# Performance work log

Hardware: AMD Instinct MI355X
Metric: run time of the kernel (lower is better)

Reference implementation:

```python
import jax, jax.numpy as jnp
import numpy as np

RH, RW = 4, 4

def window_sum(x, rh, rw):
    # cumsum along H (axis 2)
    cum_h = jnp.cumsum(x, axis=2)
    wh = 2 * rh + 1
    top = cum_h[:, :, rh:wh, :]
    midh = cum_h[:, :, wh:, :] - cum_h[:, :, :-wh, :]
    bot = cum_h[:, :, -1:, :] - cum_h[:, :, -wh:-rh - 1, :]
    out = jnp.concatenate([top, midh, bot], axis=2)
    # cumsum along W (axis 3)
    cum_w = jnp.cumsum(out, axis=3)
    ww = 2 * rw + 1
    left = cum_w[:, :, :, rw:ww]
    midw = cum_w[:, :, :, ww:] - cum_w[:, :, :, :-ww]
    right = cum_w[:, :, :, -1:] - cum_w[:, :, :, -ww:-rw - 1]
    return jnp.concatenate([left, midw, right], axis=3)


def setup_inputs() -> dict:
    key = jax.random.key(0)
    x = jax.random.normal(key, (16, 3, 1024, 1024), dtype=jnp.float32)
    return {"x": x}


def reference(x):
    win_sum = window_sum(x, RH, RW)
    count = window_sum(jnp.ones_like(x), RH, RW)
    return win_sum / count
```

## Files before the change

### kernel.cpp

```cpp
#include <hip/hip_runtime.h>

#define HH 1024
#define WW 1024
#define BH 32
#define RAD 4
#define NSTRIP (HH / BH)

typedef float vfloat4 __attribute__((ext_vector_type(4)));

struct HS { float h0, h1, h2, h3; };

__device__ __forceinline__ HS hsum_row(const float* __restrict__ row, int c,
                                       bool first, bool last) {
    float4 b = *(const float4*)(row + c);
    float4 a, d;
    if (first) a = make_float4(0.f, 0.f, 0.f, 0.f);
    else       a = *(const float4*)(row + c - 4);
    if (last)  d = make_float4(0.f, 0.f, 0.f, 0.f);
    else       d = *(const float4*)(row + c + 4);
    HS h;
    h.h0 = ((a.x + a.y) + (a.z + a.w)) + ((b.x + b.y) + (b.z + b.w)) + d.x;
    h.h1 = h.h0 - a.x + d.y;
    h.h2 = h.h1 - a.y + d.z;
    h.h3 = h.h2 - a.z + d.w;
    return h;
}

#define STEP_FAST(J) do {                                                  \
    HS h = hsum_row(rowp, c, first, last);                                 \
    vs0 += h.h0 - ring[J].h0;                                              \
    vs1 += h.h1 - ring[J].h1;                                              \
    vs2 += h.h2 - ring[J].h2;                                              \
    vs3 += h.h3 - ring[J].h3;                                              \
    ring[J] = h;                                                           \
    vfloat4 o4 = {vs0 * w0, vs1 * w1, vs2 * w2, vs3 * w3};                 \
    __builtin_nontemporal_store(o4, (vfloat4*)(op + c));                   \
    rowp += WW; op += WW;                                                  \
} while (0)

#define STEP_GEN(J) do {                                                   \
    int rl = r + RAD;                                                      \
    HS h;                                                                  \
    if (rl < HH) h = hsum_row(xin + (size_t)rl * WW, c, first, last);      \
    else { h.h0 = 0.f; h.h1 = 0.f; h.h2 = 0.f; h.h3 = 0.f; }               \
    vs0 += h.h0 - ring[J].h0;                                              \
    vs1 += h.h1 - ring[J].h1;                                              \
    vs2 += h.h2 - ring[J].h2;                                              \
    vs3 += h.h3 - ring[J].h3;                                              \
    ring[J] = h;                                                           \
    int lo = r - RAD; if (lo < 0) lo = 0;                                  \
    int hi = r + RAD; if (hi > HH - 1) hi = HH - 1;                        \
    float ich = 1.0f / (float)(hi - lo + 1);                               \
    vfloat4 o4 = {vs0 * ich * sw[0], vs1 * ich * sw[1],                    \
                  vs2 * ich * sw[2], vs3 * ich * sw[3]};                   \
    __builtin_nontemporal_store(o4, (vfloat4*)(o + (size_t)r * WW + c));   \
    ++r;                                                                   \
} while (0)

__global__ __launch_bounds__(256, 4)
void box_kernel(const float* __restrict__ x, float* __restrict__ out) {
    const int tid = threadIdx.x;

    const int lin  = blockIdx.x + NSTRIP * blockIdx.y;
    const int nblk = NSTRIP * gridDim.y;
    const int cpx  = nblk >> 3;
    const int swz  = (lin & 7) * cpx + (lin >> 3);
    const int strip = swz & (NSTRIP - 1);
    const int img   = swz / NSTRIP;

    const int r0 = strip * BH;
    const int c  = tid * 4;
    const bool first = (tid == 0);
    const bool last  = (tid == 255);

    const float* __restrict__ xin = x + (size_t)img * (HH * WW);
    float* __restrict__ o = out + (size_t)img * (HH * WW);

    float sw[4];
#pragma unroll
    for (int j = 0; j < 4; ++j) {
        int cc = c + j;
        int lo = cc - RAD < 0 ? 0 : cc - RAD;
        int hi = cc + RAD > WW - 1 ? WW - 1 : cc + RAD;
        sw[j] = 1.0f / (float)(hi - lo + 1);
    }

    HS ring[9];
    float vs0 = 0.f, vs1 = 0.f, vs2 = 0.f, vs3 = 0.f;
#pragma unroll
    for (int k = 0; k < 9; ++k) {
        int rr = r0 - RAD - 1 + k;
        HS h;
        if (rr >= 0) h = hsum_row(xin + (size_t)rr * WW, c, first, last);
        else { h.h0 = 0.f; h.h1 = 0.f; h.h2 = 0.f; h.h3 = 0.f; }
        ring[k] = h;
        vs0 += h.h0; vs1 += h.h1; vs2 += h.h2; vs3 += h.h3;
    }

    const bool interior = (r0 >= RAD) && (r0 + BH + RAD <= HH);

    if (interior) {
        const float w0 = sw[0] * (1.0f / 9.0f);
        const float w1 = sw[1] * (1.0f / 9.0f);
        const float w2 = sw[2] * (1.0f / 9.0f);
        const float w3 = sw[3] * (1.0f / 9.0f);
        const float* __restrict__ rowp = xin + (size_t)(r0 + RAD) * WW;
        float* __restrict__ op = o + (size_t)r0 * WW;
#pragma unroll 1
        for (int chunk = 0; chunk < 3; ++chunk) {
            STEP_FAST(0); STEP_FAST(1); STEP_FAST(2); STEP_FAST(3); STEP_FAST(4);
            STEP_FAST(5); STEP_FAST(6); STEP_FAST(7); STEP_FAST(8);
        }
        STEP_FAST(0); STEP_FAST(1); STEP_FAST(2); STEP_FAST(3); STEP_FAST(4);
    } else {
        int r = r0;
#pragma unroll 1
        for (int chunk = 0; chunk < 3; ++chunk) {
            STEP_GEN(0); STEP_GEN(1); STEP_GEN(2); STEP_GEN(3); STEP_GEN(4);
            STEP_GEN(5); STEP_GEN(6); STEP_GEN(7); STEP_GEN(8);
        }
        STEP_GEN(0); STEP_GEN(1); STEP_GEN(2); STEP_GEN(3); STEP_GEN(4);
    }
}

extern "C" void kernel_launch(void* const* d_in, const int* in_sizes, int n_in,
                              void* d_out, int out_size, void* d_ws, size_t ws_size,
                              hipStream_t stream) {
    const float* x = (const float*)d_in[0];
    float* out = (float*)d_out;
    int n_images = in_sizes[0] / (HH * WW);
    dim3 grid(NSTRIP, n_images);
    dim3 block(256);
    box_kernel<<<grid, block, 0, stream>>>(x, out);
}
```

Baseline: 366.5 us.

## Prefetch input rows three steps ahead and double strip height

The interior loop now loads each row three steps before it is consumed, rotating through three register sets, so global-load latency overlaps with the running vertical sum. Strip height rises from 32 to 64 rows, which reduces halo rows re-read per output row and halves the block count. Launch bounds drop to 3 waves to make room for the extra registers, and output stores become plain stores instead of nontemporal ones. The trade-offs are lower occupancy, fewer blocks to spread across CUs, and different cache behaviour for the output writes.

```diff
diff --git a/kernel.cpp b/kernel.cpp
--- a/kernel.cpp
+++ b/kernel.cpp
@@ -2,22 +2,13 @@
 
 #define HH 1024
 #define WW 1024
-#define BH 32
+#define BH 64
 #define RAD 4
 #define NSTRIP (HH / BH)
 
-typedef float vfloat4 __attribute__((ext_vector_type(4)));
-
 struct HS { float h0, h1, h2, h3; };
 
-__device__ __forceinline__ HS hsum_row(const float* __restrict__ row, int c,
-                                       bool first, bool last) {
-    float4 b = *(const float4*)(row + c);
-    float4 a, d;
-    if (first) a = make_float4(0.f, 0.f, 0.f, 0.f);
-    else       a = *(const float4*)(row + c - 4);
-    if (last)  d = make_float4(0.f, 0.f, 0.f, 0.f);
-    else       d = *(const float4*)(row + c + 4);
+__device__ __forceinline__ HS hcompute(float4 a, float4 b, float4 d) {
     HS h;
     h.h0 = ((a.x + a.y) + (a.z + a.w)) + ((b.x + b.y) + (b.z + b.w)) + d.x;
     h.h1 = h.h0 - a.x + d.y;
@@ -26,23 +17,32 @@
     return h;
 }
 
-#define STEP_FAST(J) do {                                                  \
-    HS h = hsum_row(rowp, c, first, last);                                 \
+#define LOADROW(pa, pb, pd, rowptr) do {                                   \
+    pb = *(const float4*)((rowptr) + c);                                   \
+    pa = first ? z4 : *(const float4*)((rowptr) + c - 4);                  \
+    pd = last  ? z4 : *(const float4*)((rowptr) + c + 4);                  \
+} while (0)
+
+#define PSTEP(J, PX) do {                                                  \
+    HS h = hcompute(pa##PX, pb##PX, pd##PX);                               \
+    LOADROW(pa##PX, pb##PX, pd##PX, rowp); rowp += WW;                     \
     vs0 += h.h0 - ring[J].h0;                                              \
     vs1 += h.h1 - ring[J].h1;                                              \
     vs2 += h.h2 - ring[J].h2;                                              \
     vs3 += h.h3 - ring[J].h3;                                              \
     ring[J] = h;                                                           \
-    vfloat4 o4 = {vs0 * w0, vs1 * w1, vs2 * w2, vs3 * w3};                 \
-    __builtin_nontemporal_store(o4, (vfloat4*)(op + c));                   \
-    rowp += WW; op += WW;                                                  \
+    *(float4*)(op + c) = make_float4(vs0 * w0, vs1 * w1, vs2 * w2, vs3 * w3); \
+    op += WW;                                                              \
 } while (0)
 
-#define STEP_GEN(J) do {                                                   \
+#define GSTEP(J) do {                                                      \
     int rl = r + RAD;                                                      \
     HS h;                                                                  \
-    if (rl < HH) h = hsum_row(xin + (size_t)rl * WW, c, first, last);      \
-    else { h.h0 = 0.f; h.h1 = 0.f; h.h2 = 0.f; h.h3 = 0.f; }               \
+    if (rl < HH) {                                                         \
+        float4 a, b, d;                                                    \
+        LOADROW(a, b, d, xin + (size_t)rl * WW);                           \
+        h = hcompute(a, b, d);                                             \
+    } else { h.h0 = h.h1 = h.h2 = h.h3 = 0.f; }                            \
     vs0 += h.h0 - ring[J].h0;                                              \
     vs1 += h.h1 - ring[J].h1;                                              \
     vs2 += h.h2 - ring[J].h2;                                              \
@@ -51,13 +51,13 @@
     int lo = r - RAD; if (lo < 0) lo = 0;                                  \
     int hi = r + RAD; if (hi > HH - 1) hi = HH - 1;                        \
     float ich = 1.0f / (float)(hi - lo + 1);                               \
-    vfloat4 o4 = {vs0 * ich * sw[0], vs1 * ich * sw[1],                    \
-                  vs2 * ich * sw[2], vs3 * ich * sw[3]};                   \
-    __builtin_nontemporal_store(o4, (vfloat4*)(o + (size_t)r * WW + c));   \
+    *(float4*)(o + (size_t)r * WW + c) =                                   \
+        make_float4(vs0 * ich * sw[0], vs1 * ich * sw[1],                  \
+                    vs2 * ich * sw[2], vs3 * ich * sw[3]);                 \
     ++r;                                                                   \
 } while (0)
 
-__global__ __launch_bounds__(256, 4)
+__global__ __launch_bounds__(256, 3)
 void box_kernel(const float* __restrict__ x, float* __restrict__ out) {
     const int tid = threadIdx.x;
 
@@ -72,6 +72,7 @@
     const int c  = tid * 4;
     const bool first = (tid == 0);
     const bool last  = (tid == 255);
+    const float4 z4 = make_float4(0.f, 0.f, 0.f, 0.f);
 
     const float* __restrict__ xin = x + (size_t)img * (HH * WW);
     float* __restrict__ o = out + (size_t)img * (HH * WW);
@@ -91,8 +92,11 @@
     for (int k = 0; k < 9; ++k) {
         int rr = r0 - RAD - 1 + k;
         HS h;
-        if (rr >= 0) h = hsum_row(xin + (size_t)rr * WW, c, first, last);
-        else { h.h0 = 0.f; h.h1 = 0.f; h.h2 = 0.f; h.h3 = 0.f; }
+        if (rr >= 0) {
+            float4 a, b, d;
+            LOADROW(a, b, d, xin + (size_t)rr * WW);
+            h = hcompute(a, b, d);
+        } else { h.h0 = h.h1 = h.h2 = h.h3 = 0.f; }
         ring[k] = h;
         vs0 += h.h0; vs1 += h.h1; vs2 += h.h2; vs3 += h.h3;
     }
@@ -104,22 +108,29 @@
         const float w1 = sw[1] * (1.0f / 9.0f);
         const float w2 = sw[2] * (1.0f / 9.0f);
         const float w3 = sw[3] * (1.0f / 9.0f);
-        const float* __restrict__ rowp = xin + (size_t)(r0 + RAD) * WW;
-        float* __restrict__ op = o + (size_t)r0 * WW;
+
+        float4 pa0, pb0, pd0, pa1, pb1, pd1, pa2, pb2, pd2;
+        const float* rowp = xin + (size_t)(r0 + RAD) * WW;
+        LOADROW(pa0, pb0, pd0, rowp); rowp += WW;
+        LOADROW(pa1, pb1, pd1, rowp); rowp += WW;
+        LOADROW(pa2, pb2, pd2, rowp); rowp += WW;
+
+        float* op = o + (size_t)r0 * WW;
 #pragma unroll 1
-        for (int chunk = 0; chunk < 3; ++chunk) {
-            STEP_FAST(0); STEP_FAST(1); STEP_FAST(2); STEP_FAST(3); STEP_FAST(4);
-            STEP_FAST(5); STEP_FAST(6); STEP_FAST(7); STEP_FAST(8);
+        for (int chunk = 0; chunk < 7; ++chunk) {
+            PSTEP(0, 0); PSTEP(1, 1); PSTEP(2, 2);
+            PSTEP(3, 0); PSTEP(4, 1); PSTEP(5, 2);
+            PSTEP(6, 0); PSTEP(7, 1); PSTEP(8, 2);
         }
-        STEP_FAST(0); STEP_FAST(1); STEP_FAST(2); STEP_FAST(3); STEP_FAST(4);
+        PSTEP(0, 0);
     } else {
         int r = r0;
 #pragma unroll 1
-        for (int chunk = 0; chunk < 3; ++chunk) {
-            STEP_GEN(0); STEP_GEN(1); STEP_GEN(2); STEP_GEN(3); STEP_GEN(4);
-            STEP_GEN(5); STEP_GEN(6); STEP_GEN(7); STEP_GEN(8);
+        for (int chunk = 0; chunk < 7; ++chunk) {
+            GSTEP(0); GSTEP(1); GSTEP(2); GSTEP(3); GSTEP(4);
+            GSTEP(5); GSTEP(6); GSTEP(7); GSTEP(8);
         }
-        STEP_GEN(0); STEP_GEN(1); STEP_GEN(2); STEP_GEN(3); STEP_GEN(4);
+        GSTEP(0);
     }
 }
 
```

Result: slower. 387.8 us (+5.8%).
